# Kernel tuning notes

Hardware: AMD Instinct MI355X
Metric: run time of the kernel (lower is better)

Reference implementation:

```python
import jax, jax.numpy as jnp
import numpy as np
import math

D_MODEL = 1024
N_HEADS = 16
D_K = D_MODEL // N_HEADS
THETA = 10000.0
B, S = 4, 2048


def setup_inputs() -> dict:
    key = jax.random.key(0)
    ks = jax.random.split(key, 5)
    std = math.sqrt(2.0 / (D_MODEL + D_MODEL))
    mk = lambda k: jax.random.normal(k, (D_MODEL, D_MODEL), jnp.float32) * std
    return {
        "x": jax.random.normal(ks[0], (B, S, D_MODEL), jnp.float32),
        "Wq": mk(ks[1]),
        "Wk": mk(ks[2]),
        "Wv": mk(ks[3]),
        "Wo": mk(ks[4]),
        "token_positions": jnp.arange(S, dtype=jnp.int32),
    }


def _rope(x, token_positions):
    # x: [B, H, S, d_k]; rotate adjacent pairs
    dk2 = x.shape[-1] // 2
    freqs = 1.0 / THETA ** (jnp.arange(0, x.shape[-1], 2, dtype=jnp.float32) / x.shape[-1])
    angles = token_positions.astype(jnp.float32)[:, None] * freqs[None, :]  # [S, dk2]
    cos, sin = jnp.cos(angles), jnp.sin(angles)
    xp = x.reshape(*x.shape[:-1], dk2, 2)
    x1, x2 = xp[..., 0], xp[..., 1]
    r1 = x1 * cos - x2 * sin
    r2 = x1 * sin + x2 * cos
    return jnp.stack([r1, r2], axis=-1).reshape(x.shape)


def reference(x, Wq, Wk, Wv, Wo, token_positions):
    seq_len = x.shape[-2]
    qkv_w = jnp.concatenate([Wq, Wk, Wv], axis=0)  # [3*d_model, d_model]
    qkv = x @ qkv_w.T  # [B, S, 3*d_model]
    q, k, v = jnp.split(qkv, 3, axis=-1)

    def heads(t):  # [B, S, H*dk] -> [B, H, S, dk]
        return t.reshape(*t.shape[:-1], N_HEADS, D_K).swapaxes(-3, -2)

    q, k, v = heads(q), heads(k), heads(v)
    q = _rope(q, token_positions)
    k = _rope(k, token_positions)

    scores = jnp.einsum("bhqd,bhkd->bhqk", q, k) / math.sqrt(D_K)
    causal = jnp.tril(jnp.ones((seq_len, seq_len), dtype=bool))
    scores = jnp.where(causal[None, None], scores, -jnp.inf)
    attn = jax.nn.softmax(scores, axis=-1)
    out = jnp.einsum("bhqk,bhkd->bhqd", attn, v)  # [B, H, S, dk]
    out = out.swapaxes(-3, -2).reshape(*x.shape[:-1], D_MODEL)
    return out @ Wo.T
```

## Files before the change

### kernel.cpp

```cpp
#include <hip/hip_runtime.h>
#include <hip/hip_bf16.h>


#define S_LEN 2048
#define NH 16
#define BATCH 4

typedef __bf16 bf16x8 __attribute__((ext_vector_type(8)));
typedef float f32x4 __attribute__((ext_vector_type(4)));
typedef float f32x16 __attribute__((ext_vector_type(16)));

__device__ __forceinline__ unsigned short f2bf(float f) {
  __bf16 h = (__bf16)f;
  return __builtin_bit_cast(unsigned short, h);
}
__device__ __forceinline__ float bf2f(unsigned short u) {
  return (float)__builtin_bit_cast(__bf16, u);
}

__global__ __launch_bounds__(256) void cast_bf16_kernel(const float* __restrict__ in,
                                                        unsigned short* __restrict__ out,
                                                        int n4) {
  int i = blockIdx.x * 256 + threadIdx.x;
  if (i < n4) {
    const float4 v = reinterpret_cast<const float4*>(in)[i];
    ushort4 o;
    o.x = f2bf(v.x); o.y = f2bf(v.y); o.z = f2bf(v.z); o.w = f2bf(v.w);
    reinterpret_cast<ushort4*>(out)[i] = o;
  }
}

__global__ __launch_bounds__(256) void cast_w_kernel(const float* __restrict__ Wq,
                                                     const float* __restrict__ Wk,
                                                     const float* __restrict__ Wv,
                                                     const float* __restrict__ Wo,
                                                     unsigned short* __restrict__ WQKV,
                                                     unsigned short* __restrict__ WOB) {
  int i = blockIdx.x * 256 + threadIdx.x;
  int which = i >> 18;
  int idx = i & 262143;
  const float* src = (which == 0) ? Wq : (which == 1) ? Wk : (which == 2) ? Wv : Wo;
  unsigned short* dst = (which < 3) ? (WQKV + ((size_t)which << 20)) : WOB;
  const float4 v = reinterpret_cast<const float4*>(src)[idx];
  ushort4 o;
  o.x = f2bf(v.x); o.y = f2bf(v.y); o.z = f2bf(v.z); o.w = f2bf(v.w);
  reinterpret_cast<ushort4*>(dst)[idx] = o;
}

__global__ __launch_bounds__(256) void trigf_kernel(const int* __restrict__ pos,
                                                    float* __restrict__ trigF) {
  int idx = blockIdx.x * 256 + threadIdx.x;
  int s = idx >> 5, i = idx & 31;
  float freq = expf(-0.28782313662425575f * (float)i);
  float a = (float)pos[s] * freq;
  int off = (s >> 5) * 2048 + (i >> 3) * 512 + ((((i >> 2) & 1) * 32) + (s & 31)) * 8 + 2 * (i & 3);
  trigF[off] = cosf(a);
  trigF[off + 1] = sinf(a);
}

template <int FUSED>
__global__ __launch_bounds__(256) void gemm_bt_kernel(const unsigned short* __restrict__ A,
                                                      const unsigned short* __restrict__ B,
                                                      void* __restrict__ Cv,
                                                      int M, int N, int K,
                                                      const float* __restrict__ trigF,
                                                      unsigned short* __restrict__ Qf,
                                                      unsigned short* __restrict__ Kf,
                                                      unsigned short* __restrict__ Vf) {
  __shared__ unsigned short SMEM[8192];
  unsigned short* As = SMEM;
  unsigned short* Bs = SMEM + 4096;
  const int tid = threadIdx.x;
  const int w = tid >> 6;
  const int l = tid & 63;

  const int nwg = gridDim.x * gridDim.y;
  const int bid = blockIdx.y * gridDim.x + blockIdx.x;
  const int cpx = nwg >> 3;
  const int swz = (bid & 7) * cpx + (bid >> 3);
  const int bxi = swz % gridDim.x;
  const int byi = swz / gridDim.x;

  const size_t bm = (size_t)byi * 128;
  const size_t bn = (size_t)bxi * 128;
  const int wr = (w >> 1) * 64;
  const int wc = (w & 1) * 64;

  f32x4 acc[4][4];
#pragma unroll
  for (int m = 0; m < 4; ++m)
#pragma unroll
    for (int n = 0; n < 4; ++n) acc[m][n] = (f32x4){0.f, 0.f, 0.f, 0.f};

  const int srow = w * 16 + (l >> 2);
  const int scol = (l & 3) * 8;
  const unsigned short* gA = A + (bm + srow) * K + scol;
  const unsigned short* gB = B + (bn + srow) * K + scol;
  unsigned short* lA = &As[(w * 16) * 32];
  unsigned short* lB = &Bs[(w * 16) * 32];

  const int ldm = l & 15;
  const int lg = l >> 4;
  const int ldk = lg * 8;

  for (int k0 = 0; k0 < K; k0 += 32) {
    __builtin_amdgcn_global_load_lds((const __attribute__((address_space(1))) void*)(gA + k0),
                                     (__attribute__((address_space(3))) void*)lA, 16, 0, 0);
    __builtin_amdgcn_global_load_lds((const __attribute__((address_space(1))) void*)(gA + (size_t)64 * K + k0),
                                     (__attribute__((address_space(3))) void*)(lA + 64 * 32), 16, 0, 0);
    __builtin_amdgcn_global_load_lds((const __attribute__((address_space(1))) void*)(gB + k0),
                                     (__attribute__((address_space(3))) void*)lB, 16, 0, 0);
    __builtin_amdgcn_global_load_lds((const __attribute__((address_space(1))) void*)(gB + (size_t)64 * K + k0),
                                     (__attribute__((address_space(3))) void*)(lB + 64 * 32), 16, 0, 0);
    __syncthreads();

    bf16x8 av[4], bv[4];
#pragma unroll
    for (int m = 0; m < 4; ++m)
      av[m] = *(const bf16x8*)&As[(wr + m * 16 + ldm) * 32 + ldk];
#pragma unroll
    for (int n = 0; n < 4; ++n)
      bv[n] = *(const bf16x8*)&Bs[(wc + n * 16 + ldm) * 32 + ldk];
#pragma unroll
    for (int m = 0; m < 4; ++m)
#pragma unroll
      for (int n = 0; n < 4; ++n)
        acc[m][n] = __builtin_amdgcn_mfma_f32_16x16x32_bf16(av[m], bv[n], acc[m][n], 0, 0, 0);
    __syncthreads();
  }

  if constexpr (!FUSED) {
    const size_t crow0 = bm + wr + lg * 4;
    const int ccol0 = wc + ldm;
#pragma unroll
    for (int m = 0; m < 4; ++m)
#pragma unroll
      for (int n = 0; n < 4; ++n)
#pragma unroll
        for (int i = 0; i < 4; ++i) {
          size_t idx = (crow0 + m * 16 + i) * (size_t)N + bn + ccol0 + n * 16;
          ((float*)Cv)[idx] = acc[m][n][i];
        }
  } else {
    const int cb = (int)bn + wc;
    const int region = cb >> 10;
    const int h = (cb & 1023) >> 6;
    const int rowbase0 = (int)bm + wr;
    const int bidx = rowbase0 >> 11;
    const size_t headf = ((size_t)(bidx * NH + h)) << 17;
    unsigned short* dst = (region == 0) ? Qf : (region == 1) ? Kf : Vf;
    unsigned short* scr = &SMEM[w * 1536];
    const float qsc = (region == 0) ? 0.125f : 1.0f;

#pragma unroll
    for (int m = 0; m < 4; ++m) {
      const int rowbase = rowbase0 + m * 16;
      const int st5 = (rowbase & 2047) >> 5;
      if (region < 2) {
#pragma unroll
        for (int n = 0; n < 4; ++n)
#pragma unroll
          for (int i = 0; i < 4; ++i)
            scr[(lg * 4 + i) * 72 + n * 16 + ldm] = f2bf(acc[m][n][i]);
#pragma unroll
        for (int t = 0; t < 2; ++t) {
          const int f = l + t * 64;
          const int fd = f >> 4;
          const int sl = f & 15;
          bf16x8 v = *(const bf16x8*)&scr[sl * 72 + fd * 8];
          const size_t off = (size_t)st5 * 2048 + (fd >> 1) * 512 +
                             (size_t)(((fd & 1) * 32) + ((m & 1) * 16 + sl)) * 8;
          f32x4 t0 = *(const f32x4*)&trigF[off];
          f32x4 t1 = *(const f32x4*)&trigF[off + 4];
          bf16x8 ov;
#pragma unroll
          for (int j = 0; j < 4; ++j) {
            const float c = (j < 2) ? t0[2 * j] : t1[2 * (j - 2)];
            const float s_ = (j < 2) ? t0[2 * j + 1] : t1[2 * (j - 2) + 1];
            const float x = (float)v[2 * j];
            const float y = (float)v[2 * j + 1];
            ov[2 * j] = (__bf16)((x * c - y * s_) * qsc);
            ov[2 * j + 1] = (__bf16)((x * s_ + y * c) * qsc);
          }
          *(bf16x8*)(dst + headf + off) = ov;
        }
      } else {
#pragma unroll
        for (int n = 0; n < 4; ++n)
#pragma unroll
          for (int i = 0; i < 4; ++i)
            scr[(n * 16 + ldm) * 24 + lg * 4 + i] = f2bf(acc[m][n][i]);
#pragma unroll
        for (int t = 0; t < 2; ++t) {
          const int sh = t;
          const int dd = l;
          bf16x8 v = *(const bf16x8*)&scr[dd * 24 + sh * 8];
          const size_t off = (size_t)st5 * 2048 + (dd >> 5) * 1024 + (m & 1) * 512 +
                             (size_t)(sh * 32 + (dd & 31)) * 8;
          *(bf16x8*)(dst + headf + off) = v;
        }
      }
    }
  }
}

__global__ __launch_bounds__(256) void attn_kernel(const unsigned short* __restrict__ Qf,
                                                   const unsigned short* __restrict__ Kf,
                                                   const unsigned short* __restrict__ Vf,
                                                   unsigned short* __restrict__ att) {
  __shared__ float comb[2][64][36];
  const int l = threadIdx.x & 63;
  const int w = threadIdx.x >> 6;
  const int lq = l & 31;
  const int hi = l >> 5;

  const int i = blockIdx.x;
  const int xcd = i & 7;
  const int r = i >> 3;
  const int hd = (xcd << 3) | (r & 7);
  const int rr = r >> 3;
  const int b = hd >> 4, h = hd & 15;

  const int p = w >> 1;
  const int s_half = w & 1;
  const int qt = p ? (63 - rr) : rr;

  const size_t headf = (size_t)(b * NH + h) << 17;
  const int q = qt * 32 + lq;

  bf16x8 qf[4];
  {
    const unsigned short* qp = Qf + headf + (size_t)qt * 2048 + l * 8;
#pragma unroll
    for (int m = 0; m < 4; ++m) qf[m] = *(const bf16x8*)(qp + m * 512);
  }
  float l_run = 0.f;
  f32x16 o0, o1;
#pragma unroll
  for (int i2 = 0; i2 < 16; ++i2) { o0[i2] = 0.f; o1[i2] = 0.f; }

  const unsigned short* kbase = Kf + headf + l * 8;
  const unsigned short* vbase = Vf + headf + l * 8;

  for (int nt = s_half; nt <= qt; nt += 2) {
    f32x16 s;
#pragma unroll
    for (int i2 = 0; i2 < 16; ++i2) s[i2] = 0.f;
    const unsigned short* kp = kbase + (size_t)nt * 2048;
#pragma unroll
    for (int m = 0; m < 4; ++m)
      s = __builtin_amdgcn_mfma_f32_32x32x16_bf16(*(const bf16x8*)(kp + m * 512), qf[m], s, 0, 0, 0);

    float pr[16];
    if (nt == qt) {
#pragma unroll
      for (int r2 = 0; r2 < 16; ++r2) {
        const int key = nt * 32 + (r2 & 3) + 8 * (r2 >> 2) + 4 * hi;
        pr[r2] = (key <= q) ? __expf(s[r2] - 4.0f) : 0.f;
      }
    } else {
#pragma unroll
      for (int r2 = 0; r2 < 16; ++r2) pr[r2] = __expf(s[r2] - 4.0f);
    }
#pragma unroll
    for (int r2 = 0; r2 < 16; ++r2) l_run += pr[r2];

    unsigned int pw[8];
#pragma unroll
    for (int t = 0; t < 8; ++t)
      asm("v_cvt_pk_bf16_f32 %0, %1, %2" : "=v"(pw[t]) : "v"(pr[2 * t]), "v"(pr[2 * t + 1]));
    auto r0 = __builtin_amdgcn_permlane32_swap(pw[0], pw[2], false, false);
    auto r1 = __builtin_amdgcn_permlane32_swap(pw[1], pw[3], false, false);
    auto r2 = __builtin_amdgcn_permlane32_swap(pw[4], pw[6], false, false);
    auto r3 = __builtin_amdgcn_permlane32_swap(pw[5], pw[7], false, false);
    union { unsigned int u[4]; bf16x8 v; } pb0, pb1;
    pb0.u[0] = r0[0]; pb0.u[1] = r1[0]; pb0.u[2] = r0[1]; pb0.u[3] = r1[1];
    pb1.u[0] = r2[0]; pb1.u[1] = r3[0]; pb1.u[2] = r2[1]; pb1.u[3] = r3[1];

    const unsigned short* vp = vbase + (size_t)nt * 2048;
    o0 = __builtin_amdgcn_mfma_f32_32x32x16_bf16(*(const bf16x8*)(vp), pb0.v, o0, 0, 0, 0);
    o0 = __builtin_amdgcn_mfma_f32_32x32x16_bf16(*(const bf16x8*)(vp + 512), pb1.v, o0, 0, 0, 0);
    o1 = __builtin_amdgcn_mfma_f32_32x32x16_bf16(*(const bf16x8*)(vp + 1024), pb0.v, o1, 0, 0, 0);
    o1 = __builtin_amdgcn_mfma_f32_32x32x16_bf16(*(const bf16x8*)(vp + 1536), pb1.v, o1, 0, 0, 0);
  }

  if (s_half) {
    float* dst = &comb[p][l][0];
#pragma unroll
    for (int jj = 0; jj < 4; ++jj) {
      *(f32x4*)(dst + 4 * jj) = (f32x4){o0[4 * jj], o0[4 * jj + 1], o0[4 * jj + 2], o0[4 * jj + 3]};
      *(f32x4*)(dst + 16 + 4 * jj) = (f32x4){o1[4 * jj], o1[4 * jj + 1], o1[4 * jj + 2], o1[4 * jj + 3]};
    }
    dst[32] = l_run;
  }
  __syncthreads();
  if (!s_half) {
    const float* src = &comb[p][l][0];
#pragma unroll
    for (int jj = 0; jj < 4; ++jj) {
      f32x4 a = *(const f32x4*)(src + 4 * jj);
      f32x4 c = *(const f32x4*)(src + 16 + 4 * jj);
#pragma unroll
      for (int t = 0; t < 4; ++t) { o0[4 * jj + t] += a[t]; o1[4 * jj + t] += c[t]; }
    }
    l_run += src[32];
    const float l_tot = l_run + __shfl_xor(l_run, 32, 64);
    const float inv = 1.f / l_tot;
    unsigned short* op = att + (size_t)(b * S_LEN + q) * 1024 + h * 64;
#pragma unroll
    for (int jj = 0; jj < 4; ++jj) {
      ushort4 v0, v1;
      v0.x = f2bf(o0[4 * jj + 0] * inv); v0.y = f2bf(o0[4 * jj + 1] * inv);
      v0.z = f2bf(o0[4 * jj + 2] * inv); v0.w = f2bf(o0[4 * jj + 3] * inv);
      *(ushort4*)(op + 8 * jj + 4 * hi) = v0;
      v1.x = f2bf(o1[4 * jj + 0] * inv); v1.y = f2bf(o1[4 * jj + 1] * inv);
      v1.z = f2bf(o1[4 * jj + 2] * inv); v1.w = f2bf(o1[4 * jj + 3] * inv);
      *(ushort4*)(op + 32 + 8 * jj + 4 * hi) = v1;
    }
  }
}

extern "C" void kernel_launch(void* const* d_in, const int* in_sizes, int n_in,
                              void* d_out, int out_size, void* d_ws, size_t ws_size,
                              hipStream_t stream) {
  const float* x  = (const float*)d_in[0];
  const float* Wq = (const float*)d_in[1];
  const float* Wk = (const float*)d_in[2];
  const float* Wv = (const float*)d_in[3];
  const float* Wo = (const float*)d_in[4];
  const int* pos  = (const int*)d_in[5];
  float* out = (float*)d_out;

  char* ws = (char*)d_ws;
  unsigned short* XB   = (unsigned short*)(ws + 0);
  unsigned short* WQKV = (unsigned short*)(ws + 16777216);
  unsigned short* WOB  = (unsigned short*)(ws + 23068672);
  unsigned short* QF   = (unsigned short*)(ws + 75497472);
  unsigned short* KF   = (unsigned short*)(ws + 92274688);
  unsigned short* VF   = (unsigned short*)(ws + 109051904);
  unsigned short* ATT  = (unsigned short*)(ws + 125829120);
  float* TRIGF         = (float*)(ws + 142606336);

  cast_bf16_kernel<<<8192, 256, 0, stream>>>(x, XB, 2097152);
  cast_w_kernel<<<4096, 256, 0, stream>>>(Wq, Wk, Wv, Wo, WQKV, WOB);
  trigf_kernel<<<256, 256, 0, stream>>>(pos, TRIGF);

  gemm_bt_kernel<1><<<dim3(24, 64), 256, 0, stream>>>(XB, WQKV, nullptr, 8192, 3072, 1024,
                                                      TRIGF, QF, KF, VF);

  attn_kernel<<<2048, 256, 0, stream>>>(QF, KF, VF, ATT);

  gemm_bt_kernel<0><<<dim3(8, 64), 256, 0, stream>>>(ATT, WOB, out, 8192, 1024, 1024,
                                                     nullptr, nullptr, nullptr, nullptr);
}
```

Before: 275.9 us.

## Deepen GEMM K-tile to 64 and software-pipeline QK with softmax-PV in attention

The GEMM now stages a 64-wide K slice per iteration, doubling LDS to 32KB and halving the number of barrier pairs per output tile. The attention loop is restructured so the QK^T MFMAs for the next key tile are issued before the exp/convert/PV work of the current tile. This lets matrix-core work overlap with the VALU softmax and the global loads. The costs are higher register pressure (two live score accumulators) and more LDS per block, which may reduce occupancy.

```diff
diff --git a/kernel.cpp b/kernel.cpp
--- a/kernel.cpp
+++ b/kernel.cpp
@@ -67,9 +67,9 @@
                                                       unsigned short* __restrict__ Qf,
                                                       unsigned short* __restrict__ Kf,
                                                       unsigned short* __restrict__ Vf) {
-  __shared__ unsigned short SMEM[8192];
+  __shared__ unsigned short SMEM[16384];
   unsigned short* As = SMEM;
-  unsigned short* Bs = SMEM + 4096;
+  unsigned short* Bs = SMEM + 8192;
   const int tid = threadIdx.x;
   const int w = tid >> 6;
   const int l = tid & 63;
@@ -92,40 +92,41 @@
 #pragma unroll
     for (int n = 0; n < 4; ++n) acc[m][n] = (f32x4){0.f, 0.f, 0.f, 0.f};
 
-  const int srow = w * 16 + (l >> 2);
-  const int scol = (l & 3) * 8;
+  const int srow = w * 8 + (l >> 3);
+  const int scol = (l & 7) * 8;
   const unsigned short* gA = A + (bm + srow) * K + scol;
   const unsigned short* gB = B + (bn + srow) * K + scol;
-  unsigned short* lA = &As[(w * 16) * 32];
-  unsigned short* lB = &Bs[(w * 16) * 32];
 
   const int ldm = l & 15;
   const int lg = l >> 4;
-  const int ldk = lg * 8;
-
-  for (int k0 = 0; k0 < K; k0 += 32) {
-    __builtin_amdgcn_global_load_lds((const __attribute__((address_space(1))) void*)(gA + k0),
-                                     (__attribute__((address_space(3))) void*)lA, 16, 0, 0);
-    __builtin_amdgcn_global_load_lds((const __attribute__((address_space(1))) void*)(gA + (size_t)64 * K + k0),
-                                     (__attribute__((address_space(3))) void*)(lA + 64 * 32), 16, 0, 0);
-    __builtin_amdgcn_global_load_lds((const __attribute__((address_space(1))) void*)(gB + k0),
-                                     (__attribute__((address_space(3))) void*)lB, 16, 0, 0);
-    __builtin_amdgcn_global_load_lds((const __attribute__((address_space(1))) void*)(gB + (size_t)64 * K + k0),
-                                     (__attribute__((address_space(3))) void*)(lB + 64 * 32), 16, 0, 0);
+
+  for (int k0 = 0; k0 < K; k0 += 64) {
+#pragma unroll
+    for (int j = 0; j < 4; ++j) {
+      __builtin_amdgcn_global_load_lds(
+          (const __attribute__((address_space(1))) void*)(gA + (size_t)j * 32 * K + k0),
+          (__attribute__((address_space(3))) void*)&As[j * 2048 + w * 512], 16, 0, 0);
+      __builtin_amdgcn_global_load_lds(
+          (const __attribute__((address_space(1))) void*)(gB + (size_t)j * 32 * K + k0),
+          (__attribute__((address_space(3))) void*)&Bs[j * 2048 + w * 512], 16, 0, 0);
+    }
     __syncthreads();
 
-    bf16x8 av[4], bv[4];
-#pragma unroll
-    for (int m = 0; m < 4; ++m)
-      av[m] = *(const bf16x8*)&As[(wr + m * 16 + ldm) * 32 + ldk];
-#pragma unroll
-    for (int n = 0; n < 4; ++n)
-      bv[n] = *(const bf16x8*)&Bs[(wc + n * 16 + ldm) * 32 + ldk];
-#pragma unroll
-    for (int m = 0; m < 4; ++m)
+#pragma unroll
+    for (int kk = 0; kk < 2; ++kk) {
+      bf16x8 av[4], bv[4];
+#pragma unroll
+      for (int m = 0; m < 4; ++m)
+        av[m] = *(const bf16x8*)&As[(wr + m * 16 + ldm) * 64 + kk * 32 + lg * 8];
 #pragma unroll
       for (int n = 0; n < 4; ++n)
-        acc[m][n] = __builtin_amdgcn_mfma_f32_16x16x32_bf16(av[m], bv[n], acc[m][n], 0, 0, 0);
+        bv[n] = *(const bf16x8*)&Bs[(wc + n * 16 + ldm) * 64 + kk * 32 + lg * 8];
+#pragma unroll
+      for (int m = 0; m < 4; ++m)
+#pragma unroll
+        for (int n = 0; n < 4; ++n)
+          acc[m][n] = __builtin_amdgcn_mfma_f32_16x16x32_bf16(av[m], bv[n], acc[m][n], 0, 0, 0);
+    }
     __syncthreads();
   }
 
@@ -228,11 +229,11 @@
   const size_t headf = (size_t)(b * NH + h) << 17;
   const int q = qt * 32 + lq;
 
-  bf16x8 qf[4];
+  bf16x8 qfr[4];
   {
     const unsigned short* qp = Qf + headf + (size_t)qt * 2048 + l * 8;
 #pragma unroll
-    for (int m = 0; m < 4; ++m) qf[m] = *(const bf16x8*)(qp + m * 512);
+    for (int m = 0; m < 4; ++m) qfr[m] = *(const bf16x8*)(qp + m * 512);
   }
   float l_run = 0.f;
   f32x16 o0, o1;
@@ -242,15 +243,17 @@
   const unsigned short* kbase = Kf + headf + l * 8;
   const unsigned short* vbase = Vf + headf + l * 8;
 
-  for (int nt = s_half; nt <= qt; nt += 2) {
+  auto QK = [&](int nt) -> f32x16 {
     f32x16 s;
 #pragma unroll
     for (int i2 = 0; i2 < 16; ++i2) s[i2] = 0.f;
     const unsigned short* kp = kbase + (size_t)nt * 2048;
 #pragma unroll
     for (int m = 0; m < 4; ++m)
-      s = __builtin_amdgcn_mfma_f32_32x32x16_bf16(*(const bf16x8*)(kp + m * 512), qf[m], s, 0, 0, 0);
-
+      s = __builtin_amdgcn_mfma_f32_32x32x16_bf16(*(const bf16x8*)(kp + m * 512), qfr[m], s, 0, 0, 0);
+    return s;
+  };
+  auto PROCESS = [&](const f32x16& s, int nt) {
     float pr[16];
     if (nt == qt) {
 #pragma unroll
@@ -269,19 +272,38 @@
 #pragma unroll
     for (int t = 0; t < 8; ++t)
       asm("v_cvt_pk_bf16_f32 %0, %1, %2" : "=v"(pw[t]) : "v"(pr[2 * t]), "v"(pr[2 * t + 1]));
-    auto r0 = __builtin_amdgcn_permlane32_swap(pw[0], pw[2], false, false);
-    auto r1 = __builtin_amdgcn_permlane32_swap(pw[1], pw[3], false, false);
-    auto r2 = __builtin_amdgcn_permlane32_swap(pw[4], pw[6], false, false);
-    auto r3 = __builtin_amdgcn_permlane32_swap(pw[5], pw[7], false, false);
+    auto x0 = __builtin_amdgcn_permlane32_swap(pw[0], pw[2], false, false);
+    auto x1 = __builtin_amdgcn_permlane32_swap(pw[1], pw[3], false, false);
+    auto x2 = __builtin_amdgcn_permlane32_swap(pw[4], pw[6], false, false);
+    auto x3 = __builtin_amdgcn_permlane32_swap(pw[5], pw[7], false, false);
     union { unsigned int u[4]; bf16x8 v; } pb0, pb1;
-    pb0.u[0] = r0[0]; pb0.u[1] = r1[0]; pb0.u[2] = r0[1]; pb0.u[3] = r1[1];
-    pb1.u[0] = r2[0]; pb1.u[1] = r3[0]; pb1.u[2] = r2[1]; pb1.u[3] = r3[1];
+    pb0.u[0] = x0[0]; pb0.u[1] = x1[0]; pb0.u[2] = x0[1]; pb0.u[3] = x1[1];
+    pb1.u[0] = x2[0]; pb1.u[1] = x3[0]; pb1.u[2] = x2[1]; pb1.u[3] = x3[1];
 
     const unsigned short* vp = vbase + (size_t)nt * 2048;
     o0 = __builtin_amdgcn_mfma_f32_32x32x16_bf16(*(const bf16x8*)(vp), pb0.v, o0, 0, 0, 0);
     o0 = __builtin_amdgcn_mfma_f32_32x32x16_bf16(*(const bf16x8*)(vp + 512), pb1.v, o0, 0, 0, 0);
     o1 = __builtin_amdgcn_mfma_f32_32x32x16_bf16(*(const bf16x8*)(vp + 1024), pb0.v, o1, 0, 0, 0);
     o1 = __builtin_amdgcn_mfma_f32_32x32x16_bf16(*(const bf16x8*)(vp + 1536), pb1.v, o1, 0, 0, 0);
+  };
+
+  int nt = s_half;
+  if (nt <= qt) {
+    f32x16 sA = QK(nt);
+    f32x16 sB;
+    while (true) {
+      const int ntB = nt + 2;
+      const bool hasB = (ntB <= qt);
+      if (hasB) sB = QK(ntB);
+      PROCESS(sA, nt);
+      if (!hasB) break;
+      const int ntC = ntB + 2;
+      const bool hasC = (ntC <= qt);
+      if (hasC) sA = QK(ntC);
+      PROCESS(sB, ntB);
+      if (!hasC) break;
+      nt = ntC;
+    }
   }
 
   if (s_half) {
```

New measurement: 347.1 us. 25.8% more time.
